# Kernel optimization log

Hardware: AMD Instinct MI355X
Metric: run time of the kernel (lower is better)

## Reference

```python
import jax, jax.numpy as jnp
import numpy as np

COMMITMENT_COST = 0.25


def setup_inputs() -> dict:
    key = jax.random.key(0)
    k1, k2 = jax.random.split(key)
    inputs = jax.random.normal(k1, (32, 64, 64, 64), dtype=jnp.float32)  # (B, D, H, W)
    codewords = jax.random.uniform(k2, (512, 64), dtype=jnp.float32)    # (K, D)
    return {"inputs": inputs, "codewords": codewords}


def reference(inputs, codewords):
    # NCHW -> NHWC so last dim is codewords_dim
    x = jnp.transpose(inputs, (0, 2, 3, 1))          # (B, H, W, D)
    B, H, W, D = x.shape
    flat = x.reshape(-1, D)                          # (N, D)

    x_sq = jnp.sum(flat * flat, axis=1, keepdims=True)            # (N, 1)
    c_sq = jnp.sum(codewords * codewords, axis=1)[None, :]        # (1, K)
    dots = flat @ codewords.T                                     # (N, K)
    distances = x_sq + c_sq - 2.0 * dots                          # (N, K)

    encoding_indices = jnp.argmin(distances, axis=1)              # (N,)
    quantized = codewords[encoding_indices].reshape(B, H, W, D)   # (B, H, W, D)

    quantizing_loss = jnp.mean((jax.lax.stop_gradient(quantized) - x) ** 2)
    commitment_loss = jnp.mean((quantized - jax.lax.stop_gradient(x)) ** 2)
    loss = quantizing_loss + COMMITMENT_COST * commitment_loss

    # straight-through estimator
    quantized_st = x + jax.lax.stop_gradient(quantized - x)

    out = jnp.transpose(quantized_st, (0, 3, 1, 2))               # (B, D, H, W)
    return out, encoding_indices.reshape(B, H, W), loss
```

## Files before the change

kernel.cpp:

```cpp
#include <hip/hip_runtime.h>
#include <math.h>

#define HWSZ 4096
#define DIM  64
#define KCW  512
#define NROW 131072
#define CMAX 16
#define XPW  33
#define WVS  2464

typedef short bf16x8 __attribute__((ext_vector_type(8)));
typedef float f32x4  __attribute__((ext_vector_type(4)));

#define WS_CSQ  64
#define WS_BLOB 1024
#define WS_PART 17408

static __device__ __forceinline__ unsigned short f2bf(float f) {
    union { float f; unsigned u; } v; v.f = f;
    unsigned u = v.u;
    return (unsigned short)((u + 0x7fffu + ((u >> 16) & 1u)) >> 16);
}

__global__ void vq_prep_kernel(const float* __restrict__ cw, float* __restrict__ ws) {
    int tg = blockIdx.x * 256 + threadIdx.x;
    if (tg < KCW) {
        const float4* c4 = (const float4*)(cw + (size_t)tg * DIM);
        float s0 = 0.f, s1 = 0.f, s2 = 0.f, s3 = 0.f;
        #pragma unroll
        for (int i = 0; i < 16; ++i) {
            float4 c = c4[i];
            s0 = fmaf(c.x, c.x, s0); s1 = fmaf(c.y, c.y, s1);
            s2 = fmaf(c.z, c.z, s2); s3 = fmaf(c.w, c.w, s3);
        }
        ws[WS_CSQ + tg] = (s0 + s1) + (s2 + s3);
    }
    if (tg < 4096) {
        int l = tg & 63, f = (tg >> 6) & 1, kt = tg >> 7;
        int col = kt * 16 + (l & 15);
        unsigned short* blob = (unsigned short*)(ws + WS_BLOB);
        #pragma unroll
        for (int j = 0; j < 8; ++j) {
            int d = f * 32 + (l >> 4) * 8 + j;
            blob[((kt * 2 + f) * 64 + l) * 8 + j] = f2bf(cw[col * DIM + d]);
        }
    }
}

__global__ __attribute__((amdgpu_flat_work_group_size(256, 256), amdgpu_waves_per_eu(4, 4)))
void vq_main_kernel(const float* __restrict__ in, const float* __restrict__ cw,
                    const float* __restrict__ ws_ro, float* __restrict__ part,
                    float* __restrict__ out) {
    __shared__ float lds[4 * WVS];

    const int t  = threadIdx.x;
    const int w  = t >> 6, l = t & 63;
    const int hi = l >> 4, cl = l & 15;

    float* S     = lds + w * WVS;
    float* xw    = S;
    float* xsq   = S + 2112;
    int*   sidxp = (int*)(S + 2144);
    int*   cntsp = (int*)(S + 2176);
    unsigned short* candp = (unsigned short*)(S + 2208);

    const int b    = blockIdx.x >> 5;
    const int hwW  = (blockIdx.x & 31) * 128 + w * 32;
    const int rowW = blockIdx.x * 128 + w * 32;

    if (l < 32) cntsp[l] = 0;

    const float* __restrict__ xg = in + (size_t)b * (DIM * HWSZ) + hwW;
    {
        const int dd2 = l >> 5, hw = l & 31;
        #pragma unroll
        for (int i = 0; i < 32; ++i) {
            int d = 2 * i + dd2;
            xw[d * XPW + hw] = xg[(size_t)d * HWSZ + hw];
        }
    }

    if (l < 32) {
        float s = 0.f;
        for (int d = 0; d < DIM; ++d) { float xv = xw[d * XPW + l]; s = fmaf(xv, xv, s); }
        xsq[l] = s;
    }

    bf16x8 a00, a01, a10, a11;
    #pragma unroll
    for (int j = 0; j < 8; ++j) {
        a00[j] = (short)f2bf(-xw[(hi * 8 + j) * XPW + cl]);
        a01[j] = (short)f2bf(-xw[(32 + hi * 8 + j) * XPW + cl]);
        a10[j] = (short)f2bf(-xw[(hi * 8 + j) * XPW + 16 + cl]);
        a11[j] = (short)f2bf(-xw[(32 + hi * 8 + j) * XPW + 16 + cl]);
    }

    const bf16x8* __restrict__ bp   = (const bf16x8*)(ws_ro + WS_BLOB);
    const float*  __restrict__ csqg = ws_ro + WS_CSQ;

    float mn0[4] = {INFINITY, INFINITY, INFINITY, INFINITY};
    float mn1[4] = {INFINITY, INFINITY, INFINITY, INFINITY};
    #pragma unroll 2
    for (int kt = 0; kt < 32; ++kt) {
        float ci = 0.5f * csqg[kt * 16 + cl];
        bf16x8 b0 = bp[(kt * 2 + 0) * 64 + l];
        bf16x8 b1 = bp[(kt * 2 + 1) * 64 + l];
        f32x4 acc0 = {ci, ci, ci, ci};
        f32x4 acc1 = {ci, ci, ci, ci};
        acc0 = __builtin_amdgcn_mfma_f32_16x16x32_bf16(a00, b0, acc0, 0, 0, 0);
        acc0 = __builtin_amdgcn_mfma_f32_16x16x32_bf16(a01, b1, acc0, 0, 0, 0);
        acc1 = __builtin_amdgcn_mfma_f32_16x16x32_bf16(a10, b0, acc1, 0, 0, 0);
        acc1 = __builtin_amdgcn_mfma_f32_16x16x32_bf16(a11, b1, acc1, 0, 0, 0);
        #pragma unroll
        for (int rg = 0; rg < 4; ++rg) {
            mn0[rg] = fminf(mn0[rg], acc0[rg]);
            mn1[rg] = fminf(mn1[rg], acc1[rg]);
        }
    }
    #pragma unroll
    for (int off = 1; off < 16; off <<= 1)
        #pragma unroll
        for (int rg = 0; rg < 4; ++rg) {
            mn0[rg] = fminf(mn0[rg], __shfl_xor(mn0[rg], off, 64));
            mn1[rg] = fminf(mn1[rg], __shfl_xor(mn1[rg], off, 64));
        }

    float thr0[4], thr1[4];
    #pragma unroll
    for (int rg = 0; rg < 4; ++rg) {
        thr0[rg] = mn0[rg] + 0.0625f * sqrtf(xsq[4 * hi + rg]) + 0.03125f;
        thr1[rg] = mn1[rg] + 0.0625f * sqrtf(xsq[16 + 4 * hi + rg]) + 0.03125f;
    }

    #pragma unroll 2
    for (int kt = 0; kt < 32; ++kt) {
        float ci = 0.5f * csqg[kt * 16 + cl];
        bf16x8 b0 = bp[(kt * 2 + 0) * 64 + l];
        bf16x8 b1 = bp[(kt * 2 + 1) * 64 + l];
        f32x4 acc0 = {ci, ci, ci, ci};
        f32x4 acc1 = {ci, ci, ci, ci};
        acc0 = __builtin_amdgcn_mfma_f32_16x16x32_bf16(a00, b0, acc0, 0, 0, 0);
        acc0 = __builtin_amdgcn_mfma_f32_16x16x32_bf16(a01, b1, acc0, 0, 0, 0);
        acc1 = __builtin_amdgcn_mfma_f32_16x16x32_bf16(a10, b0, acc1, 0, 0, 0);
        acc1 = __builtin_amdgcn_mfma_f32_16x16x32_bf16(a11, b1, acc1, 0, 0, 0);
        #pragma unroll
        for (int rg = 0; rg < 4; ++rg) {
            if (acc0[rg] <= thr0[rg]) {
                int r = 4 * hi + rg;
                int pos = atomicAdd(&cntsp[r], 1);
                if (pos < CMAX) candp[r * 16 + pos] = (unsigned short)(kt * 16 + cl);
            }
            if (acc1[rg] <= thr1[rg]) {
                int r = 16 + 4 * hi + rg;
                int pos = atomicAdd(&cntsp[r], 1);
                if (pos < CMAX) candp[r * 16 + pos] = (unsigned short)(kt * 16 + cl);
            }
        }
    }

    {
        const int r = l >> 1, q = l & 1;
        const int n = cntsp[r];
        if (n <= CMAX) {
            float bb = INFINITY; int bkk = 0x7fffffff;
            const float xsqe = xsq[r];
            for (int s = q; s < n; s += 2) {
                int k = candp[r * 16 + s];
                const float4* __restrict__ c4 = (const float4*)(cw + (size_t)k * DIM);
                float d0 = 0.f, d1 = 0.f, d2 = 0.f, d3 = 0.f;
                #pragma unroll
                for (int i = 0; i < 16; ++i) {
                    float4 c = c4[i];
                    d0 = fmaf(xw[(4 * i + 0) * XPW + r], c.x, d0);
                    d1 = fmaf(xw[(4 * i + 1) * XPW + r], c.y, d1);
                    d2 = fmaf(xw[(4 * i + 2) * XPW + r], c.z, d2);
                    d3 = fmaf(xw[(4 * i + 3) * XPW + r], c.w, d3);
                }
                float dot  = (d0 + d1) + (d2 + d3);
                float dist = (xsqe + csqg[k]) - 2.f * dot;
                if (dist < bb || (dist == bb && k < bkk)) { bb = dist; bkk = k; }
            }
            {
                float ob = __shfl_xor(bb, 1, 64);
                int   ok = __shfl_xor(bkk, 1, 64);
                if (ob < bb || (ob == bb && ok < bkk)) { bb = ob; bkk = ok; }
            }
            if (q == 0) {
                sidxp[r] = bkk;
                out[(size_t)NROW * DIM + rowW + r] = (float)bkk;
            }
        }
    }

    for (int r = 0; r < 32; ++r) {
        if (cntsp[r] <= CMAX) continue;
        const float xsqe = xsq[r];
        float bb = INFINITY; int bkk = 0x7fffffff;
        for (int kk = 0; kk < 8; ++kk) {
            int k = kk * 64 + l;
            const float4* __restrict__ c4 = (const float4*)(cw + (size_t)k * DIM);
            float d0 = 0.f, d1 = 0.f, d2 = 0.f, d3 = 0.f;
            #pragma unroll
            for (int i = 0; i < 16; ++i) {
                float4 c = c4[i];
                d0 = fmaf(xw[(4 * i + 0) * XPW + r], c.x, d0);
                d1 = fmaf(xw[(4 * i + 1) * XPW + r], c.y, d1);
                d2 = fmaf(xw[(4 * i + 2) * XPW + r], c.z, d2);
                d3 = fmaf(xw[(4 * i + 3) * XPW + r], c.w, d3);
            }
            float dot  = (d0 + d1) + (d2 + d3);
            float dist = (xsqe + csqg[k]) - 2.f * dot;
            if (dist < bb || (dist == bb && k < bkk)) { bb = dist; bkk = k; }
        }
        #pragma unroll
        for (int off = 32; off; off >>= 1) {
            float ob = __shfl_down(bb, off, 64);
            int   ok = __shfl_down(bkk, off, 64);
            if (ob < bb || (ob == bb && ok < bkk)) { bb = ob; bkk = ok; }
        }
        if (l == 0) {
            sidxp[r] = bkk;
            out[(size_t)NROW * DIM + rowW + r] = (float)bkk;
        }
    }

    {
        const int r = l >> 1, q2 = l & 1;
        const int kwin = sidxp[r];
        const float4* __restrict__ qp = (const float4*)(cw + (size_t)kwin * DIM + q2 * 32);
        float* __restrict__ obase = out + (size_t)b * (DIM * HWSZ) + hwW + r;
        float lsum = 0.f;
        #pragma unroll
        for (int dd = 0; dd < 8; ++dd) {
            float4 q4 = qp[dd];
            float qv[4] = {q4.x, q4.y, q4.z, q4.w};
            #pragma unroll
            for (int c = 0; c < 4; ++c) {
                int d = q2 * 32 + dd * 4 + c;
                float xv = xw[d * XPW + r];
                obase[(size_t)d * HWSZ] = qv[c];
                float diff = qv[c] - xv;
                lsum = fmaf(diff, diff, lsum);
            }
        }
        #pragma unroll
        for (int off = 32; off; off >>= 1) lsum += __shfl_down(lsum, off, 64);
        if (l == 0) part[blockIdx.x * 4 + w] = lsum;
    }
}

__global__ void vq_finalize_kernel(const float* __restrict__ part, float* __restrict__ out) {
    __shared__ float wsum[4];
    const int t = threadIdx.x;
    float s = 0.f;
    #pragma unroll
    for (int i = 0; i < 16; ++i) s += part[t * 16 + i];
    #pragma unroll
    for (int off = 32; off; off >>= 1) s += __shfl_down(s, off, 64);
    if ((t & 63) == 0) wsum[t >> 6] = s;
    __syncthreads();
    if (t == 0)
        out[(size_t)NROW * DIM + NROW] =
            1.25f * ((wsum[0] + wsum[1]) + (wsum[2] + wsum[3])) / (float)((size_t)NROW * DIM);
}

extern "C" void kernel_launch(void* const* d_in, const int* in_sizes, int n_in,
                              void* d_out, int out_size, void* d_ws, size_t ws_size,
                              hipStream_t stream) {
    const float* in = (const float*)d_in[0];
    const float* cw = (const float*)d_in[1];
    float* out = (float*)d_out;
    float* ws  = (float*)d_ws;

    hipLaunchKernelGGL(vq_prep_kernel, dim3(16), dim3(256), 0, stream, cw, ws);
    hipLaunchKernelGGL(vq_main_kernel, dim3(NROW / 128), dim3(256), 0, stream,
                       in, cw, ws, ws + WS_PART, out);
    hipLaunchKernelGGL(vq_finalize_kernel, dim3(1), dim3(256), 0, stream, ws + WS_PART, out);
}
```

Measured before the change: 72.31 us.

## Stage bf16 codebook blob in LDS and read activations directly from global

Doubles the block to 512 threads (8 waves, 256 rows) and copies the pre-packed bf16 codebook blob and codeword norms into shared memory once per block, so both MFMA passes read B fragments from LDS instead of global/L2. The per-wave transposed activation tile in LDS is removed; activations are re-read from global memory with strided accesses in the norm, fragment build, rescoring and loss phases. This trades LDS occupancy (64KB blob per block) and extra uncoalesced or redundant global reads of x for cheaper codebook access. The partial sum layout is adjusted to 8 per block.

```diff
diff --git a/kernel.cpp b/kernel.cpp
--- a/kernel.cpp
+++ b/kernel.cpp
@@ -6,8 +6,6 @@
 #define KCW  512
 #define NROW 131072
 #define CMAX 16
-#define XPW  33
-#define WVS  2464
 
 typedef short bf16x8 __attribute__((ext_vector_type(8)));
 typedef float f32x4  __attribute__((ext_vector_type(4)));
@@ -47,64 +45,62 @@
     }
 }
 
-__global__ __attribute__((amdgpu_flat_work_group_size(256, 256), amdgpu_waves_per_eu(4, 4)))
+__global__ __launch_bounds__(512, 4)
 void vq_main_kernel(const float* __restrict__ in, const float* __restrict__ cw,
                     const float* __restrict__ ws_ro, float* __restrict__ part,
                     float* __restrict__ out) {
-    __shared__ float lds[4 * WVS];
+    __shared__ __align__(16) unsigned short blob_l[4096 * 8];
+    __shared__ float csq_l[KCW];
+    __shared__ float xsqa[8][32];
+    __shared__ int   sidxa[8][32];
+    __shared__ int   cntsa[8][32];
+    __shared__ unsigned short canda[8][32][CMAX];
 
     const int t  = threadIdx.x;
     const int w  = t >> 6, l = t & 63;
     const int hi = l >> 4, cl = l & 15;
 
-    float* S     = lds + w * WVS;
-    float* xw    = S;
-    float* xsq   = S + 2112;
-    int*   sidxp = (int*)(S + 2144);
-    int*   cntsp = (int*)(S + 2176);
-    unsigned short* candp = (unsigned short*)(S + 2208);
-
-    const int b    = blockIdx.x >> 5;
-    const int hwW  = (blockIdx.x & 31) * 128 + w * 32;
-    const int rowW = blockIdx.x * 128 + w * 32;
-
-    if (l < 32) cntsp[l] = 0;
+    const int b    = blockIdx.x >> 4;
+    const int hwW  = (blockIdx.x & 15) * 256 + w * 32;
+    const int rowW = blockIdx.x * 256 + w * 32;
+
+    {
+        const float4* __restrict__ bg = (const float4*)(ws_ro + WS_BLOB);
+        float4* bl4 = (float4*)blob_l;
+        #pragma unroll
+        for (int i = 0; i < 8; ++i) bl4[i * 512 + t] = bg[i * 512 + t];
+        csq_l[t] = ws_ro[WS_CSQ + t];
+    }
+    if (l < 32) cntsa[w][l] = 0;
 
     const float* __restrict__ xg = in + (size_t)b * (DIM * HWSZ) + hwW;
-    {
-        const int dd2 = l >> 5, hw = l & 31;
-        #pragma unroll
-        for (int i = 0; i < 32; ++i) {
-            int d = 2 * i + dd2;
-            xw[d * XPW + hw] = xg[(size_t)d * HWSZ + hw];
-        }
-    }
 
     if (l < 32) {
         float s = 0.f;
-        for (int d = 0; d < DIM; ++d) { float xv = xw[d * XPW + l]; s = fmaf(xv, xv, s); }
-        xsq[l] = s;
+        for (int d = 0; d < DIM; ++d) { float xv = xg[(size_t)d * HWSZ + l]; s = fmaf(xv, xv, s); }
+        xsqa[w][l] = s;
     }
 
     bf16x8 a00, a01, a10, a11;
     #pragma unroll
     for (int j = 0; j < 8; ++j) {
-        a00[j] = (short)f2bf(-xw[(hi * 8 + j) * XPW + cl]);
-        a01[j] = (short)f2bf(-xw[(32 + hi * 8 + j) * XPW + cl]);
-        a10[j] = (short)f2bf(-xw[(hi * 8 + j) * XPW + 16 + cl]);
-        a11[j] = (short)f2bf(-xw[(32 + hi * 8 + j) * XPW + 16 + cl]);
-    }
-
-    const bf16x8* __restrict__ bp   = (const bf16x8*)(ws_ro + WS_BLOB);
-    const float*  __restrict__ csqg = ws_ro + WS_CSQ;
+        a00[j] = (short)f2bf(-xg[(size_t)(hi * 8 + j) * HWSZ + cl]);
+        a01[j] = (short)f2bf(-xg[(size_t)(32 + hi * 8 + j) * HWSZ + cl]);
+        a10[j] = (short)f2bf(-xg[(size_t)(hi * 8 + j) * HWSZ + 16 + cl]);
+        a11[j] = (short)f2bf(-xg[(size_t)(32 + hi * 8 + j) * HWSZ + 16 + cl]);
+    }
+
+    __syncthreads();
+
+    const bf16x8* __restrict__ bls = (const bf16x8*)blob_l;
 
     float mn0[4] = {INFINITY, INFINITY, INFINITY, INFINITY};
     float mn1[4] = {INFINITY, INFINITY, INFINITY, INFINITY};
     #pragma unroll 2
     for (int kt = 0; kt < 32; ++kt) {
-        float ci = 0.5f * csqg[kt * 16 + cl];
-        bf16x8 b0 = bp[(kt * 2 + 0) * 64 + l];
-        bf16x8 b1 = bp[(kt * 2 + 1) * 64 + l];
+        float ci = 0.5f * csq_l[kt * 16 + cl];
+        bf16x8 b0 = bls[(kt * 2 + 0) * 64 + l];
+        bf16x8 b1 = bls[(kt * 2 + 1) * 64 + l];
         f32x4 acc0 = {ci, ci, ci, ci};
         f32x4 acc1 = {ci, ci, ci, ci};
         acc0 = __builtin_amdgcn_mfma_f32_16x16x32_bf16(a00, b0, acc0, 0, 0, 0);
@@ -128,15 +124,15 @@
     float thr0[4], thr1[4];
     #pragma unroll
     for (int rg = 0; rg < 4; ++rg) {
-        thr0[rg] = mn0[rg] + 0.0625f * sqrtf(xsq[4 * hi + rg]) + 0.03125f;
-        thr1[rg] = mn1[rg] + 0.0625f * sqrtf(xsq[16 + 4 * hi + rg]) + 0.03125f;
+        thr0[rg] = mn0[rg] + 0.0625f * sqrtf(xsqa[w][4 * hi + rg]) + 0.03125f;
+        thr1[rg] = mn1[rg] + 0.0625f * sqrtf(xsqa[w][16 + 4 * hi + rg]) + 0.03125f;
     }
 
     #pragma unroll 2
     for (int kt = 0; kt < 32; ++kt) {
-        float ci = 0.5f * csqg[kt * 16 + cl];
-        bf16x8 b0 = bp[(kt * 2 + 0) * 64 + l];
-        bf16x8 b1 = bp[(kt * 2 + 1) * 64 + l];
+        float ci = 0.5f * csq_l[kt * 16 + cl];
+        bf16x8 b0 = bls[(kt * 2 + 0) * 64 + l];
+        bf16x8 b1 = bls[(kt * 2 + 1) * 64 + l];
         f32x4 acc0 = {ci, ci, ci, ci};
         f32x4 acc1 = {ci, ci, ci, ci};
         acc0 = __builtin_amdgcn_mfma_f32_16x16x32_bf16(a00, b0, acc0, 0, 0, 0);
@@ -147,37 +143,38 @@
         for (int rg = 0; rg < 4; ++rg) {
             if (acc0[rg] <= thr0[rg]) {
                 int r = 4 * hi + rg;
-                int pos = atomicAdd(&cntsp[r], 1);
-                if (pos < CMAX) candp[r * 16 + pos] = (unsigned short)(kt * 16 + cl);
+                int pos = atomicAdd(&cntsa[w][r], 1);
+                if (pos < CMAX) canda[w][r][pos] = (unsigned short)(kt * 16 + cl);
             }
             if (acc1[rg] <= thr1[rg]) {
                 int r = 16 + 4 * hi + rg;
-                int pos = atomicAdd(&cntsp[r], 1);
-                if (pos < CMAX) candp[r * 16 + pos] = (unsigned short)(kt * 16 + cl);
+                int pos = atomicAdd(&cntsa[w][r], 1);
+                if (pos < CMAX) canda[w][r][pos] = (unsigned short)(kt * 16 + cl);
             }
         }
     }
 
     {
         const int r = l >> 1, q = l & 1;
-        const int n = cntsp[r];
+        const int n = cntsa[w][r];
+        const float* __restrict__ xr = xg + r;
         if (n <= CMAX) {
             float bb = INFINITY; int bkk = 0x7fffffff;
-            const float xsqe = xsq[r];
+            const float xsqe = xsqa[w][r];
             for (int s = q; s < n; s += 2) {
-                int k = candp[r * 16 + s];
+                int k = canda[w][r][s];
                 const float4* __restrict__ c4 = (const float4*)(cw + (size_t)k * DIM);
                 float d0 = 0.f, d1 = 0.f, d2 = 0.f, d3 = 0.f;
                 #pragma unroll
                 for (int i = 0; i < 16; ++i) {
                     float4 c = c4[i];
-                    d0 = fmaf(xw[(4 * i + 0) * XPW + r], c.x, d0);
-                    d1 = fmaf(xw[(4 * i + 1) * XPW + r], c.y, d1);
-                    d2 = fmaf(xw[(4 * i + 2) * XPW + r], c.z, d2);
-                    d3 = fmaf(xw[(4 * i + 3) * XPW + r], c.w, d3);
+                    d0 = fmaf(xr[(size_t)(4 * i + 0) * HWSZ], c.x, d0);
+                    d1 = fmaf(xr[(size_t)(4 * i + 1) * HWSZ], c.y, d1);
+                    d2 = fmaf(xr[(size_t)(4 * i + 2) * HWSZ], c.z, d2);
+                    d3 = fmaf(xr[(size_t)(4 * i + 3) * HWSZ], c.w, d3);
                 }
                 float dot  = (d0 + d1) + (d2 + d3);
-                float dist = (xsqe + csqg[k]) - 2.f * dot;
+                float dist = (xsqe + csq_l[k]) - 2.f * dot;
                 if (dist < bb || (dist == bb && k < bkk)) { bb = dist; bkk = k; }
             }
             {
@@ -186,15 +183,16 @@
                 if (ob < bb || (ob == bb && ok < bkk)) { bb = ob; bkk = ok; }
             }
             if (q == 0) {
-                sidxp[r] = bkk;
+                sidxa[w][r] = bkk;
                 out[(size_t)NROW * DIM + rowW + r] = (float)bkk;
             }
         }
     }
 
     for (int r = 0; r < 32; ++r) {
-        if (cntsp[r] <= CMAX) continue;
-        const float xsqe = xsq[r];
+        if (cntsa[w][r] <= CMAX) continue;
+        const float xsqe = xsqa[w][r];
+        const float* __restrict__ xr = xg + r;
         float bb = INFINITY; int bkk = 0x7fffffff;
         for (int kk = 0; kk < 8; ++kk) {
             int k = kk * 64 + l;
@@ -203,13 +201,13 @@
             #pragma unroll
             for (int i = 0; i < 16; ++i) {
                 float4 c = c4[i];
-                d0 = fmaf(xw[(4 * i + 0) * XPW + r], c.x, d0);
-                d1 = fmaf(xw[(4 * i + 1) * XPW + r], c.y, d1);
-                d2 = fmaf(xw[(4 * i + 2) * XPW + r], c.z, d2);
-                d3 = fmaf(xw[(4 * i + 3) * XPW + r], c.w, d3);
+                d0 = fmaf(xr[(size_t)(4 * i + 0) * HWSZ], c.x, d0);
+                d1 = fmaf(xr[(size_t)(4 * i + 1) * HWSZ], c.y, d1);
+                d2 = fmaf(xr[(size_t)(4 * i + 2) * HWSZ], c.z, d2);
+                d3 = fmaf(xr[(size_t)(4 * i + 3) * HWSZ], c.w, d3);
             }
             float dot  = (d0 + d1) + (d2 + d3);
-            float dist = (xsqe + csqg[k]) - 2.f * dot;
+            float dist = (xsqe + csq_l[k]) - 2.f * dot;
             if (dist < bb || (dist == bb && k < bkk)) { bb = dist; bkk = k; }
         }
         #pragma unroll
@@ -219,15 +217,16 @@
             if (ob < bb || (ob == bb && ok < bkk)) { bb = ob; bkk = ok; }
         }
         if (l == 0) {
-            sidxp[r] = bkk;
+            sidxa[w][r] = bkk;
             out[(size_t)NROW * DIM + rowW + r] = (float)bkk;
         }
     }
 
     {
         const int r = l >> 1, q2 = l & 1;
-        const int kwin = sidxp[r];
+        const int kwin = sidxa[w][r];
         const float4* __restrict__ qp = (const float4*)(cw + (size_t)kwin * DIM + q2 * 32);
+        const float* __restrict__ xe = xg + r;
         float* __restrict__ obase = out + (size_t)b * (DIM * HWSZ) + hwW + r;
         float lsum = 0.f;
         #pragma unroll
@@ -237,7 +236,7 @@
             #pragma unroll
             for (int c = 0; c < 4; ++c) {
                 int d = q2 * 32 + dd * 4 + c;
-                float xv = xw[d * XPW + r];
+                float xv = xe[(size_t)d * HWSZ];
                 obase[(size_t)d * HWSZ] = qv[c];
                 float diff = qv[c] - xv;
                 lsum = fmaf(diff, diff, lsum);
@@ -245,7 +244,7 @@
         }
         #pragma unroll
         for (int off = 32; off; off >>= 1) lsum += __shfl_down(lsum, off, 64);
-        if (l == 0) part[blockIdx.x * 4 + w] = lsum;
+        if (l == 0) part[blockIdx.x * 8 + w] = lsum;
     }
 }
 
@@ -273,7 +272,7 @@
     float* ws  = (float*)d_ws;
 
     hipLaunchKernelGGL(vq_prep_kernel, dim3(16), dim3(256), 0, stream, cw, ws);
-    hipLaunchKernelGGL(vq_main_kernel, dim3(NROW / 128), dim3(256), 0, stream,
+    hipLaunchKernelGGL(vq_main_kernel, dim3(NROW / 256), dim3(512), 0, stream,
                        in, cw, ws, ws + WS_PART, out);
     hipLaunchKernelGGL(vq_finalize_kernel, dim3(1), dim3(256), 0, stream, ws + WS_PART, out);
 }
```

New measurement: 66.06 us. 1.09x faster.
